# Performance work log

Hardware: AMD Instinct MI355X
Metric: run time of the kernel (lower is better)

Reference implementation:

```python
import jax, jax.numpy as jnp
import numpy as np

K = 1.0          # Lorentz curvature param: x_t^2 - |x_s|^2 = K
SQRT_K = 1.0
EPS = 1e-8
HEADS = 12

def add_time(s):
    t = jnp.sqrt(K + jnp.sum(s * s, axis=-1, keepdims=True))
    return jnp.concatenate([t, s], axis=-1)

def lorentz_ln(x, g, b):
    s = x[..., 1:]
    mu = jnp.mean(s, axis=-1, keepdims=True)
    var = jnp.var(s, axis=-1, keepdims=True)
    s = (s - mu) / jnp.sqrt(var + 1e-5) * g + b
    return add_time(s)

def lorentz_fc(x, W, heads=None, act=None):
    # linear on full Lorentz vector -> space part; time recomputed to stay on manifold
    s = x @ W.T
    if act is not None:
        s = act(s)
    if heads is not None:
        bsz, n, dt = s.shape
        s = s.reshape(bsz, n, heads, dt // heads).transpose(0, 2, 1, 3)  # (b,h,n,hd)
    return add_time(s)

def logmap0(x):
    t, s = x[..., :1], x[..., 1:]
    sn = jnp.sqrt(jnp.sum(s * s, axis=-1, keepdims=True))
    dist = SQRT_K * jnp.arccosh(jnp.maximum(t / SQRT_K, 1.0 + 1e-7))
    u = dist * s / jnp.maximum(sn, EPS)
    return jnp.concatenate([jnp.zeros_like(t), u], axis=-1)

def expmap0(u):
    us = u[..., 1:]
    n = jnp.sqrt(jnp.sum(us * us, axis=-1, keepdims=True))
    nc = jnp.maximum(n, EPS)
    t = SQRT_K * jnp.cosh(n / SQRT_K)
    s = SQRT_K * jnp.sinh(n / SQRT_K) * us / nc
    return jnp.concatenate([t, s], axis=-1)

def ste_clip(x, lo, hi):
    # straight-through estimator: clamp in fwd, identity grad
    return x + jax.lax.stop_gradient(jnp.clip(x, lo, hi) - x)

def ste_max_clamp(x, hi):
    return x + jax.lax.stop_gradient(jnp.minimum(x, hi) - x)

def mha_last_layer(x, Wq, Wk, Wv, Wo, alpha_raw, tau_raw, lambda_raw):
    q = lorentz_fc(x, Wq, heads=HEADS)   # (b,h,n,hd+1)
    k = lorentz_fc(x, Wk, heads=HEADS)
    v = lorentz_fc(x, Wv, heads=HEADS)
    q_t, q_s = q[..., :1], q[..., 1:]
    k_t, k_s = k[..., :1], k[..., 1:]
    # Lorentzian inner product -> hyperbolic pairwise distances
    inner_QK = -q_t @ jnp.swapaxes(k_t, -1, -2) + jnp.einsum('bhid,bhjd->bhij', q_s, k_s)
    raw_cosh = jnp.maximum(-inner_QK / K, 1.0)                # (b,h,n,n)
    is_self = raw_cosh < 1.0 + 1e-5
    safe_cosh = jnp.where(is_self, 2.0, raw_cosh)
    dist_QK = SQRT_K * jnp.arccosh(safe_cosh)
    cosh_OQ = jnp.maximum(q_t / SQRT_K, 1.0 + 1e-7)
    cosh_OK = jnp.maximum(k_t / SQRT_K, 1.0 + 1e-7)
    c_tilde = jnp.minimum(SQRT_K * jnp.arccosh(cosh_OQ), 40.0) / SQRT_K  # (b,h,n,1)
    sinh_QK = jnp.sinh(dist_QK / SQRT_K)
    sinh_OQ = jnp.sinh(c_tilde)
    numer = raw_cosh * cosh_OQ - jnp.swapaxes(cosh_OK, -1, -2)
    raw_Z = numer / (sinh_OQ * sinh_QK)
    Z_safe = jnp.where(is_self, 1.0, ste_clip(raw_Z, -1.0, 1.0))
    alpha = jax.nn.softplus(alpha_raw)
    B = alpha * c_tilde / (1.0 + alpha * c_tilde)
    lam = jax.nn.softplus(lambda_raw)
    d_L = ste_max_clamp(dist_QK, 40.0)   # float32 branch of STE_Dist_Clamp
    log_dist_penalty = -lam * jnp.log1p(d_L * d_L)
    m = 0.1
    entail = jax.nn.softplus(B + Z_safe - m) - jax.nn.softplus(jnp.asarray(-m, B.dtype))
    tau = jax.nn.softplus(tau_raw)
    score = jax.nn.softmax(log_dist_penalty - tau * entail, axis=-1)
    # expmap aggregation: tangent-space weighted mean
    v_tan = logmap0(v)
    agg = jnp.einsum('bhij,bhjd->bhid', score, v_tan)
    agg = agg / (jnp.sum(score, axis=-1, keepdims=True) + 1e-8)
    attn = expmap0(agg).transpose(0, 2, 1, 3)   # (b,n,h,hd+1)
    bsz, n, h, _ = attn.shape
    attn_s = attn[..., 1:].reshape(bsz, n, -1)
    attn_t = attn[..., :1].reshape(bsz, n, -1)
    t_new = jnp.sqrt(jnp.sum(attn_t ** 2, axis=-1, keepdims=True) - (h - 1) * K)
    return lorentz_fc(jnp.concatenate([t_new, attn_s], axis=-1), Wo)


def setup_inputs() -> dict:
    key = jax.random.key(0)
    ks = jax.random.split(key, 8)
    b, n, hidden, mlp_hidden = 4, 1024, 769, 3073
    d = hidden - 1
    xs = jax.random.normal(ks[0], (b, n, d), jnp.float32)
    x = add_time(xs)
    def w(k, o, i):
        return jax.random.normal(k, (o, i), jnp.float32) * (i ** -0.5)
    return {
        'x': x,
        'Wq': w(ks[1], d, hidden), 'Wk': w(ks[2], d, hidden), 'Wv': w(ks[3], d, hidden),
        'Wo': w(ks[4], d, hidden),
        'ln1_g': jnp.ones((d,), jnp.float32), 'ln1_b': jnp.zeros((d,), jnp.float32),
        'ln2_g': jnp.ones((d,), jnp.float32), 'ln2_b': jnp.zeros((d,), jnp.float32),
        'Wm1': w(ks[5], mlp_hidden - 1, hidden), 'Wm2': w(ks[6], d, mlp_hidden),
        'alpha_raw': jnp.zeros((1,), jnp.float32),
        'tau_raw': jnp.zeros((1,), jnp.float32),
        'lambda_raw': jnp.zeros((1,), jnp.float32),
    }


def reference(x, Wq, Wk, Wv, Wo, ln1_g, ln1_b, ln2_g, ln2_b, Wm1, Wm2, alpha_raw, tau_raw, lambda_raw):
    out = mha_last_layer(lorentz_ln(x, ln1_g, ln1_b), Wq, Wk, Wv, Wo, alpha_raw, tau_raw, lambda_raw)
    out = out[..., 1:] + x[..., 1:]                 # residual on space part (DropPath=identity in eval)
    h = lorentz_ln(add_time(out), ln2_g, ln2_b)
    h = lorentz_fc(h, Wm1, act=lambda z: jax.nn.gelu(z, approximate=False))
    h = lorentz_fc(h, Wm2)
    out = h[..., 1:] + out
    return add_time(out)
```

## Files before the change

### kernel.cpp

```cpp
#include <hip/hip_runtime.h>
#include <cstdint>
#include <cstddef>

typedef unsigned short u16;
typedef __attribute__((ext_vector_type(8))) __bf16 bf16x8;
typedef __attribute__((ext_vector_type(4))) float f32x4;

#define SEQ 1024
#define MROWS 4096
#define DDIM 768
#define HID 769
#define KP1 800
#define MLPD 3072
#define KP2 3104
#define NHEADS 12
#define LN2F 0.69314718056f
#define LOG2EF 1.44269504089f

static __device__ __forceinline__ u16 f2bf(float f){
  union { float f; uint32_t u; } v; v.f = f;
  return (u16)((v.u + 0x7FFFu + ((v.u >> 16) & 1u)) >> 16);
}

static __device__ __forceinline__ f32x4 mfma16(bf16x8 a, bf16x8 b, f32x4 c){
  return __builtin_amdgcn_mfma_f32_16x16x32_bf16(a, b, c, 0, 0, 0);
}

static __device__ __forceinline__ void async_lds16(const u16* g, u16* l){
  u16* gm = const_cast<u16*>(g);
  __builtin_amdgcn_global_load_lds(
      (__attribute__((address_space(1))) void*)gm,
      (__attribute__((address_space(3))) void*)l, 16, 0, 0);
}

static __device__ __forceinline__ float blk_reduce(float v, float* red, int tid){
  #pragma unroll
  for (int off = 1; off < 64; off <<= 1) v += __shfl_xor(v, off, 64);
  __syncthreads();
  if ((tid & 63) == 0) red[tid >> 6] = v;
  __syncthreads();
  return red[0] + red[1] + red[2] + red[3];
}

static __device__ __forceinline__ void conv_seg(const float* W, u16* O, int idx, int K, int Kp){
  int n = idx / Kp, k = idx - n * Kp;
  O[idx] = (k < K) ? f2bf(W[(size_t)n * K + k]) : (u16)0;
}
__global__ __launch_bounds__(256) void conv_all(const float* __restrict__ Wq, const float* __restrict__ Wk,
    const float* __restrict__ Wv, const float* __restrict__ Wo,
    const float* __restrict__ Wm1, const float* __restrict__ Wm2, u16* __restrict__ dst){
  int b = blockIdx.x, tid = threadIdx.x;
  if (b < 2400){        conv_seg(Wq,  dst,            b*256+tid,        769, 800); }
  else if (b < 4800){   conv_seg(Wk,  dst + 614400,  (b-2400)*256+tid,  769, 800); }
  else if (b < 7200){   conv_seg(Wv,  dst + 1228800, (b-4800)*256+tid,  769, 800); }
  else if (b < 9600){   conv_seg(Wo,  dst + 1843200, (b-7200)*256+tid,  769, 800); }
  else if (b < 19200){  conv_seg(Wm1, dst + 2457600, (b-9600)*256+tid,  769, 800); }
  else {                conv_seg(Wm2, dst + 4915200, (b-19200)*256+tid, 3073, 3104); }
}

__global__ __launch_bounds__(256) void ln_kernel(const float* __restrict__ X, int xstr, int xoff,
    const float* __restrict__ g, const float* __restrict__ b, u16* __restrict__ O){
  __shared__ float red[4];
  int m = blockIdx.x, tid = threadIdx.x;
  const float* xr = X + (size_t)m * xstr + xoff;
  float s[3], y[3];
  float s1 = 0.f, s2 = 0.f;
  #pragma unroll
  for (int j = 0; j < 3; j++){ float v = xr[tid + j*256]; s[j] = v; s1 += v; s2 += v*v; }
  s1 = blk_reduce(s1, red, tid);
  s2 = blk_reduce(s2, red, tid);
  float mu = s1 * (1.f/768.f);
  float var = s2 * (1.f/768.f) - mu*mu;
  float rstd = rsqrtf(var + 1e-5f);
  float q = 0.f;
  #pragma unroll
  for (int j = 0; j < 3; j++){ int i = tid + j*256; y[j] = (s[j]-mu)*rstd*g[i] + b[i]; q += y[j]*y[j]; }
  q = blk_reduce(q, red, tid);
  u16* orow = O + (size_t)m * KP1;
  #pragma unroll
  for (int j = 0; j < 3; j++) orow[1 + tid + j*256] = f2bf(y[j]);
  if (tid == 0) orow[0] = f2bf(sqrtf(1.f + q));
  if (tid < 31) orow[769 + tid] = 0;
}

__global__ __launch_bounds__(256) void ln_sum_kernel(const float* __restrict__ P4,
    const float* __restrict__ x, const float* __restrict__ g, const float* __restrict__ b,
    float* __restrict__ out1, u16* __restrict__ O){
  __shared__ float red[4];
  int m = blockIdx.x, tid = threadIdx.x;
  float s[3], y[3];
  float s1 = 0.f, s2 = 0.f;
  #pragma unroll
  for (int j = 0; j < 3; j++){
    int col = tid + j*256;
    float v = x[(size_t)m * HID + 1 + col];
    #pragma unroll
    for (int z = 0; z < 4; z++) v += P4[(size_t)z*MROWS*DDIM + (size_t)m*DDIM + col];
    out1[(size_t)m*DDIM + col] = v;
    s[j] = v; s1 += v; s2 += v*v;
  }
  s1 = blk_reduce(s1, red, tid);
  s2 = blk_reduce(s2, red, tid);
  float mu = s1 * (1.f/768.f);
  float var = s2 * (1.f/768.f) - mu*mu;
  float rstd = rsqrtf(var + 1e-5f);
  float q = 0.f;
  #pragma unroll
  for (int j = 0; j < 3; j++){ int i = tid + j*256; y[j] = (s[j]-mu)*rstd*g[i] + b[i]; q += y[j]*y[j]; }
  q = blk_reduce(q, red, tid);
  u16* orow = O + (size_t)m * KP1;
  #pragma unroll
  for (int j = 0; j < 3; j++) orow[1 + tid + j*256] = f2bf(y[j]);
  if (tid == 0) orow[0] = f2bf(sqrtf(1.f + q));
  if (tid < 31) orow[769 + tid] = 0;
}

__global__ __launch_bounds__(256) void gemm_qkv(
    const u16* __restrict__ A,
    const u16* __restrict__ B0, const u16* __restrict__ B1, const u16* __restrict__ B2,
    float* __restrict__ C, int N, int Kp)
{
  __shared__ u16 As[128*32];
  __shared__ u16 Bs[128*32];
  int tid = threadIdx.x;
  int wave = tid >> 6, lane = tid & 63;
  int lrow = lane & 15, lq = lane >> 4;
  int m0 = blockIdx.y * 128, n0 = blockIdx.x * 128;
  int wm = wave >> 1, wn = wave & 1;
  const u16* B = (blockIdx.z == 0) ? B0 : (blockIdx.z == 1 ? B1 : B2);
  C += (size_t)blockIdx.z * MROWS * N;
  f32x4 acc[4][4] = {};
  int seg = wave * 2;
  int srow = lane >> 2;
  int scol = (lane & 3) * 8;
  const u16* Abase = A + (size_t)m0 * Kp;
  const u16* Bbase = B + (size_t)n0 * Kp;
  for (int k0 = 0; k0 < Kp; k0 += 32){
    __syncthreads();
    #pragma unroll
    for (int i = 0; i < 2; i++){
      int s = seg + i;
      async_lds16(Abase + (size_t)(s*16 + srow) * Kp + k0 + scol, As + s*512);
      async_lds16(Bbase + (size_t)(s*16 + srow) * Kp + k0 + scol, Bs + s*512);
    }
    __syncthreads();
    bf16x8 af[4], bfr[4];
    #pragma unroll
    for (int t = 0; t < 4; t++){
      af[t]  = *(const bf16x8*)(As + (wm*64 + t*16 + lrow)*32 + lq*8);
      bfr[t] = *(const bf16x8*)(Bs + (wn*64 + t*16 + lrow)*32 + lq*8);
    }
    #pragma unroll
    for (int mt = 0; mt < 4; mt++)
      #pragma unroll
      for (int nt = 0; nt < 4; nt++)
        acc[mt][nt] = mfma16(af[mt], bfr[nt], acc[mt][nt]);
  }
  #pragma unroll
  for (int mt = 0; mt < 4; mt++)
    #pragma unroll
    for (int nt = 0; nt < 4; nt++){
      int col = n0 + wn*64 + nt*16 + lrow;
      #pragma unroll
      for (int r = 0; r < 4; r++){
        int row = m0 + wm*64 + mt*16 + lq*4 + r;
        C[(size_t)row * N + col] = acc[mt][nt][r];
      }
    }
}

__global__ __launch_bounds__(256) void gemm_split(
    const u16* __restrict__ A, const u16* __restrict__ B, float* __restrict__ C,
    int N, int Kp)
{
  __shared__ u16 As[128*32];
  __shared__ u16 Bs[128*32];
  int tid = threadIdx.x;
  int wave = tid >> 6, lane = tid & 63;
  int lrow = lane & 15, lq = lane >> 4;
  int m0 = blockIdx.y * 128, n0 = blockIdx.x * 128;
  int wm = wave >> 1, wn = wave & 1;
  int chunks = Kp >> 5;
  int nz = gridDim.z, z = blockIdx.z;
  int base = chunks / nz, rem = chunks - base * nz;
  int begin = z * base + (z < rem ? z : rem);
  int count = base + (z < rem ? 1 : 0);
  C += (size_t)z * MROWS * N;
  f32x4 acc[4][4] = {};
  int seg = wave * 2;
  int srow = lane >> 2;
  int scol = (lane & 3) * 8;
  const u16* Abase = A + (size_t)m0 * Kp;
  const u16* Bbase = B + (size_t)n0 * Kp;
  for (int kc = begin; kc < begin + count; kc++){
    int k0 = kc * 32;
    __syncthreads();
    #pragma unroll
    for (int i = 0; i < 2; i++){
      int s = seg + i;
      async_lds16(Abase + (size_t)(s*16 + srow) * Kp + k0 + scol, As + s*512);
      async_lds16(Bbase + (size_t)(s*16 + srow) * Kp + k0 + scol, Bs + s*512);
    }
    __syncthreads();
    bf16x8 af[4], bfr[4];
    #pragma unroll
    for (int t = 0; t < 4; t++){
      af[t]  = *(const bf16x8*)(As + (wm*64 + t*16 + lrow)*32 + lq*8);
      bfr[t] = *(const bf16x8*)(Bs + (wn*64 + t*16 + lrow)*32 + lq*8);
    }
    #pragma unroll
    for (int mt = 0; mt < 4; mt++)
      #pragma unroll
      for (int nt = 0; nt < 4; nt++)
        acc[mt][nt] = mfma16(af[mt], bfr[nt], acc[mt][nt]);
  }
  #pragma unroll
  for (int mt = 0; mt < 4; mt++)
    #pragma unroll
    for (int nt = 0; nt < 4; nt++){
      int col = n0 + wn*64 + nt*16 + lrow;
      #pragma unroll
      for (int r = 0; r < 4; r++){
        int row = m0 + wm*64 + mt*16 + lq*4 + r;
        C[(size_t)row * N + col] = acc[mt][nt][r];
      }
    }
}

__global__ __launch_bounds__(256) void pack_qk(const float* __restrict__ raw,
    u16* __restrict__ Qp, u16* __restrict__ Kpk, float* __restrict__ qt, float* __restrict__ kt)
{
  int wave = threadIdx.x >> 6, lane = threadIdx.x & 63;
  int m = blockIdx.x * 4 + wave;
  int h = blockIdx.y;
  int which = blockIdx.z;
  const float* src = raw + (size_t)which * MROWS * DDIM + (size_t)m * DDIM + h*64 + lane;
  float v = *src;
  float ss = v*v;
  #pragma unroll
  for (int off = 1; off < 64; off <<= 1) ss += __shfl_xor(ss, off, 64);
  int b = m >> 10, n = m & 1023, bh = b * NHEADS + h;
  u16* dst = (which ? Kpk : Qp) + ((size_t)bh * SEQ + n) * 64 + lane;
  *dst = f2bf(v);
  if (lane == 0) (which ? kt : qt)[bh * SEQ + n] = sqrtf(1.f + ss);
}

__global__ __launch_bounds__(256) void pack_v(const float* __restrict__ vraw, u16* __restrict__ Vt){
  __shared__ float part[256];
  __shared__ float scl[64];
  __shared__ float tile[64][65];
  int tid = threadIdx.x;
  int kb = blockIdx.x, bh = blockIdx.y;
  int b = bh / NHEADS, h = bh - b*NHEADS;
  int kl = tid >> 2;
  int d0 = (tid & 3) * 16;
  int m = b * SEQ + kb * 64 + kl;
  float v[16]; float ss = 0.f;
  const float* src = vraw + (size_t)m * DDIM + h*64 + d0;
  #pragma unroll
  for (int i = 0; i < 16; i++){ v[i] = src[i]; ss += v[i]*v[i]; }
  part[tid] = ss;
  __syncthreads();
  if ((tid & 3) == 0){
    float s2 = part[tid] + part[tid+1] + part[tid+2] + part[tid+3];
    float sn = sqrtf(s2);
    float tv = sqrtf(1.f + s2);
    float ctv = fmaxf(tv, 1.f + 1e-7f);
    float dist = __logf(ctv + sqrtf(fmaxf(ctv*ctv - 1.f, 0.f)));
    scl[kl] = dist / fmaxf(sn, 1e-8f);
  }
  __syncthreads();
  float sc = scl[kl];
  #pragma unroll
  for (int i = 0; i < 16; i++) tile[kl][d0 + i] = v[i] * sc;
  __syncthreads();
  int dim = tid >> 2;
  int kk0 = (tid & 3) * 16;
  u16 tmp[16];
  #pragma unroll
  for (int i = 0; i < 16; i++) tmp[i] = f2bf(tile[kk0 + i][dim]);
  u16* dst = Vt + ((size_t)bh * 64 + dim) * SEQ + kb*64 + kk0;
  *(uint4*)dst       = *(const uint4*)tmp;
  *(uint4*)(dst + 8) = *(const uint4*)(tmp + 8);
}

__global__ __launch_bounds__(256) void attn_kernel(
    const u16* __restrict__ Q, const u16* __restrict__ K, const u16* __restrict__ Vt,
    const float* __restrict__ qt, const float* __restrict__ kt,
    float* __restrict__ pAgg, float* __restrict__ pDen,
    const float* __restrict__ a_raw, const float* __restrict__ t_raw, const float* __restrict__ l_raw)
{
  __shared__ float rv[4][64];
  __shared__ u16 Pl[4][16*72];
  int tid = threadIdx.x;
  int bh = blockIdx.y, ks = blockIdx.z;
  int qbase = blockIdx.x * 64;
  float alpha = __logf(1.f + __expf(a_raw[0]));
  float tau   = __logf(1.f + __expf(t_raw[0]));
  float lam   = __logf(1.f + __expf(l_raw[0]));
  if (tid < 64){
    float qtv = qt[bh * SEQ + qbase + tid];
    float cq = fmaxf(qtv, 1.f + 1e-7f);
    float A = cq + __builtin_amdgcn_sqrtf(fmaxf(cq*cq - 1.f, 0.f));
    float ct = fminf(__builtin_amdgcn_logf(A) * LN2F, 40.f);
    float e = __expf(ct);
    float sh = 0.5f * (e - __builtin_amdgcn_rcpf(e));
    float ac = alpha * ct;
    rv[0][tid] = qtv;
    rv[1][tid] = cq;
    rv[2][tid] = __builtin_amdgcn_rcpf(sh);
    rv[3][tid] = (ac * __builtin_amdgcn_rcpf(1.f + ac) - 0.1f) * LOG2EF;
  }
  __syncthreads();
  int wave = tid >> 6, lane = tid & 63;
  int lrow = lane & 15, lq = lane >> 4;
  int myrow = wave*16 + lrow;
  float qt_l = rv[0][myrow], cq_l = rv[1][myrow], rri_l = rv[2][myrow], Bw_l = rv[3][myrow];
  const float tbase = tau * 0.92967051f;
  const u16* Qb = Q + ((size_t)bh * SEQ + qbase + wave*16 + lrow) * 64 + lq*8;
  bf16x8 bq0 = *(const bf16x8*)Qb;
  bf16x8 bq1 = *(const bf16x8*)(Qb + 32);
  const u16* Kh = K + (size_t)bh * SEQ * 64;
  const u16* Vh = Vt + (size_t)bh * 64 * SEQ;
  const float* ktp = kt + (size_t)bh * SEQ;
  u16* Pw = &Pl[wave][0];
  f32x4 o[4] = {};
  float dsum = 0.f;
  for (int jt = 0; jt < 8; jt++){
    int jbase = ks * 512 + jt * 64;
    f32x4 s[4];
    #pragma unroll
    for (int ct = 0; ct < 4; ct++){
      const u16* Ka = Kh + (size_t)(jbase + ct*16 + lrow) * 64 + lq*8;
      bf16x8 a0 = *(const bf16x8*)Ka;
      bf16x8 a1 = *(const bf16x8*)(Ka + 32);
      f32x4 z = {0.f, 0.f, 0.f, 0.f};
      z = mfma16(a0, bq0, z);
      z = mfma16(a1, bq1, z);
      s[ct] = z;
    }
    #pragma unroll
    for (int ct = 0; ct < 4; ct++){
      float4 kv = *(const float4*)(ktp + jbase + ct*16 + lq*4);
      uint32_t pu[4];
      #pragma unroll
      for (int r = 0; r < 4; r++){
        float ktv = (r == 0) ? kv.x : (r == 1) ? kv.y : (r == 2) ? kv.z : kv.w;
        float c = fmaxf(__builtin_fmaf(qt_l, ktv, -s[ct][r]), 1.f);
        bool self = c < 1.00001f;
        float ce = self ? 2.f : c;
        float cm1 = __builtin_fmaf(ce, ce, -1.f);
        float rs = __builtin_amdgcn_rsqf(cm1);
        float shq = cm1 * rs;
        float d = fminf(__builtin_amdgcn_logf(ce + shq) * LN2F, 40.f);
        float L1 = __builtin_amdgcn_logf(__builtin_fmaf(d, d, 1.f));
        float Z = __builtin_fmaf(ce, cq_l, -ktv) * rri_l * rs;
        Z = fminf(fmaxf(Z, -1.f), 1.f);
        Z = self ? 1.f : Z;
        float w2 = __builtin_fmaf(Z, LOG2EF, Bw_l);
        float ew = __builtin_amdgcn_exp2f(w2);
        float L2 = __builtin_amdgcn_logf(ew + 1.f);
        float logit = __builtin_fmaf(-lam, L1, __builtin_fmaf(-tau, L2, tbase));
        float p = __builtin_amdgcn_exp2f(logit);
        uint32_t u = __float_as_uint(p);
        pu[r] = u;
        dsum += __uint_as_float(u & 0xFFFF0000u);
      }
      uint32_t lo = __builtin_amdgcn_perm(pu[1], pu[0], 0x07060302u);
      uint32_t hi = __builtin_amdgcn_perm(pu[3], pu[2], 0x07060302u);
      uint2 pk; pk.x = lo; pk.y = hi;
      *(uint2*)(Pw + lrow*72 + ct*16 + lq*4) = pk;
    }
    bf16x8 ap0 = *(const bf16x8*)(Pw + lrow*72 + lq*8);
    bf16x8 ap1 = *(const bf16x8*)(Pw + lrow*72 + 32 + lq*8);
    #pragma unroll
    for (int nt = 0; nt < 4; nt++){
      const u16* Vb = Vh + (size_t)(nt*16 + lrow) * SEQ + jbase + lq*8;
      bf16x8 bv0 = *(const bf16x8*)Vb;
      bf16x8 bv1 = *(const bf16x8*)(Vb + 32);
      o[nt] = mfma16(ap0, bv0, o[nt]);
      o[nt] = mfma16(ap1, bv1, o[nt]);
    }
  }
  dsum += __shfl_xor(dsum, 16, 64);
  dsum += __shfl_xor(dsum, 32, 64);
  size_t pbase = ((size_t)(ks*48 + bh) * SEQ) + qbase;
  if (lq == 0) pDen[pbase + wave*16 + lrow] = dsum;
  #pragma unroll
  for (int nt = 0; nt < 4; nt++)
    #pragma unroll
    for (int r = 0; r < 4; r++)
      pAgg[(pbase + wave*16 + lq*4 + r) * 64 + nt*16 + lrow] = o[nt][r];
}

__global__ __launch_bounds__(768) void expmap_pack(const float* __restrict__ pAgg,
    const float* __restrict__ pDen, u16* __restrict__ O){
  __shared__ float th2[NHEADS];
  int m = blockIdx.x, tid = threadIdx.x;
  int h = tid >> 6, lane = tid & 63;
  int b = m >> 10, n = m & 1023, bh = b*NHEADS + h;
  size_t i0 = ((size_t)bh * SEQ + n);
  size_t i1 = ((size_t)(48 + bh) * SEQ + n);
  float d = pDen[i0] + pDen[i1];
  float rden = __builtin_amdgcn_rcpf(d * (1.f + 1e-8f));
  float u = (pAgg[i0*64 + lane] + pAgg[i1*64 + lane]) * rden;
  float n2 = u*u;
  #pragma unroll
  for (int off = 1; off < 64; off <<= 1) n2 += __shfl_xor(n2, off, 64);
  float nn = sqrtf(n2);
  float e = __expf(nn);
  float ch = 0.5f * (e + 1.f/e);
  float sh = 0.5f * (e - 1.f/e);
  float sc = sh / fmaxf(nn, 1e-8f);
  u16* orow = O + (size_t)m * KP1;
  orow[1 + h*64 + lane] = f2bf(u * sc);
  if (lane == 0) th2[h] = ch*ch;
  __syncthreads();
  if (tid == 0){
    float ssum = 0.f;
    #pragma unroll
    for (int i = 0; i < NHEADS; i++) ssum += th2[i];
    orow[0] = f2bf(sqrtf(ssum - 11.f));
  }
  if (tid >= 1 && tid < 32) orow[768 + tid] = 0;
}

__global__ __launch_bounds__(256) void gelu_pack(const float* __restrict__ Zin, u16* __restrict__ O){
  __shared__ float red[4];
  int m = blockIdx.x, tid = threadIdx.x;
  const float* zr = Zin + (size_t)m * MLPD;
  float gv[12]; float gs = 0.f;
  #pragma unroll
  for (int j = 0; j < 12; j++){
    float z = zr[tid + j*256];
    float e = 0.5f * z * (1.f + erff(z * 0.70710678f));
    gv[j] = e; gs += e*e;
  }
  gs = blk_reduce(gs, red, tid);
  u16* orow = O + (size_t)m * KP2;
  #pragma unroll
  for (int j = 0; j < 12; j++) orow[1 + tid + j*256] = f2bf(gv[j]);
  if (tid == 0) orow[0] = f2bf(sqrtf(1.f + gs));
  if (tid < 31) orow[3073 + tid] = 0;
}

__global__ __launch_bounds__(256) void final_sum(const float* __restrict__ P4,
    const float* __restrict__ out1, float* __restrict__ out){
  __shared__ float red[4];
  int m = blockIdx.x, tid = threadIdx.x;
  float v[3]; float s2 = 0.f;
  #pragma unroll
  for (int j = 0; j < 3; j++){
    int col = tid + j*256;
    float t = out1[(size_t)m*DDIM + col];
    #pragma unroll
    for (int z = 0; z < 4; z++) t += P4[(size_t)z*MROWS*DDIM + (size_t)m*DDIM + col];
    v[j] = t; s2 += t*t;
  }
  s2 = blk_reduce(s2, red, tid);
  float* orow = out + (size_t)m * HID;
  if (tid == 0) orow[0] = sqrtf(1.f + s2);
  #pragma unroll
  for (int j = 0; j < 3; j++) orow[1 + tid + j*256] = v[j];
}

extern "C" void kernel_launch(void* const* d_in, const int* in_sizes, int n_in,
                              void* d_out, int out_size, void* d_ws, size_t ws_size,
                              hipStream_t stream)
{
  (void)in_sizes; (void)n_in; (void)out_size; (void)ws_size;
  const float* x   = (const float*)d_in[0];
  const float* Wq  = (const float*)d_in[1];
  const float* Wk  = (const float*)d_in[2];
  const float* Wv  = (const float*)d_in[3];
  const float* Wo  = (const float*)d_in[4];
  const float* g1p = (const float*)d_in[5];
  const float* b1p = (const float*)d_in[6];
  const float* g2p = (const float*)d_in[7];
  const float* b2p = (const float*)d_in[8];
  const float* Wm1 = (const float*)d_in[9];
  const float* Wm2 = (const float*)d_in[10];
  const float* ar  = (const float*)d_in[11];
  const float* tr  = (const float*)d_in[12];
  const float* lr  = (const float*)d_in[13];

  char* ws = (char*)d_ws;
  u16*   wqb  = (u16*)(ws + 0);
  u16*   wkb  = (u16*)(ws + 1228800);
  u16*   wvb  = (u16*)(ws + 2457600);
  u16*   wob  = (u16*)(ws + 3686400);
  u16*   wm1b = (u16*)(ws + 4915200);
  u16*   wm2b = (u16*)(ws + 9830400);
  u16*   xln  = (u16*)(ws + 14598144);
  float* qkv  = (float*)(ws + 21151744);
  u16*   qp   = (u16*)(ws + 58900480);
  u16*   kpk  = (u16*)(ws + 65191936);
  u16*   vt   = (u16*)(ws + 71483392);
  float* qtb  = (float*)(ws + 77774848);
  float* ktb  = (float*)(ws + 77971456);
  float* pAgg = (float*)(ws + 78168064);
  float* pDen = (float*)(ws + 103333888);
  u16*   woin = (u16*)(ws + 103727104);
  float* woP  = (float*)(ws + 21151744);
  float* out1 = (float*)(ws + 78168064);
  u16*   ln2b = (u16*)(ws + 90750976);
  float* mlp1 = (float*)(ws + 21151744);
  u16*   g1b  = (u16*)(ws + 90750976);
  float* out2P= (float*)(ws + 21151744);

  conv_all<<<dim3(28512), 256, 0, stream>>>(Wq, Wk, Wv, Wo, Wm1, Wm2, wqb);
  ln_kernel<<<dim3(4096), 256, 0, stream>>>(x, 769, 1, g1p, b1p, xln);
  gemm_qkv<<<dim3(6, 32, 3), 256, 0, stream>>>(xln, wqb, wkb, wvb, qkv, 768, 800);
  pack_qk<<<dim3(1024, 12, 2), 256, 0, stream>>>(qkv, qp, kpk, qtb, ktb);
  pack_v<<<dim3(16, 48), 256, 0, stream>>>(qkv + (size_t)2*MROWS*DDIM, vt);
  attn_kernel<<<dim3(16, 48, 2), 256, 0, stream>>>(qp, kpk, vt, qtb, ktb, pAgg, pDen, ar, tr, lr);
  expmap_pack<<<dim3(4096), 768, 0, stream>>>(pAgg, pDen, woin);
  gemm_split<<<dim3(6, 32, 4), 256, 0, stream>>>(woin, wob, woP, 768, 800);
  ln_sum_kernel<<<dim3(4096), 256, 0, stream>>>(woP, x, g2p, b2p, out1, ln2b);
  gemm_split<<<dim3(24, 32, 1), 256, 0, stream>>>(ln2b, wm1b, mlp1, 3072, 800);
  gelu_pack<<<dim3(4096), 256, 0, stream>>>(mlp1, g1b);
  gemm_split<<<dim3(6, 32, 4), 256, 0, stream>>>(g1b, wm2b, out2P, 768, 3104);
  final_sum<<<dim3(4096), 256, 0, stream>>>(out2P, out1, (float*)d_out);
}
```

Measured before the change: 424.7 us.

## Fuse QKV into one GEMM, split attention K four ways, feed P via registers

Replaces the three-way QKV GEMM with a single gemm_split over the concatenated weights, writing a row-interleaved 2304-wide output that the pack kernels now read with the new stride. The attention key range is split into four partitions instead of two, for more blocks and parallelism, with partial results spread across two workspace buffers. The P·V product now uses the 16x16x16 bf16 MFMA with P kept in registers, removing the per-wave LDS staging, and partial outputs are stored as float4. The distance clamp at 40 is dropped, expmap_pack sums four partials, and the workspace layout is reshuffled, which risks buffer overlap and more partial-sum traffic.

```diff
diff --git a/kernel.cpp b/kernel.cpp
--- a/kernel.cpp
+++ b/kernel.cpp
@@ -5,6 +5,7 @@
 typedef unsigned short u16;
 typedef __attribute__((ext_vector_type(8))) __bf16 bf16x8;
 typedef __attribute__((ext_vector_type(4))) float f32x4;
+typedef __attribute__((ext_vector_type(4))) short s16x4;
 
 #define SEQ 1024
 #define MROWS 4096
@@ -26,6 +27,14 @@
   return __builtin_amdgcn_mfma_f32_16x16x32_bf16(a, b, c, 0, 0, 0);
 }
 
+static __device__ __forceinline__ f32x4 mfma16k(s16x4 a, s16x4 b, f32x4 c){
+  return __builtin_amdgcn_mfma_f32_16x16x16bf16_1k(a, b, c, 0, 0, 0);
+}
+
+static __device__ __forceinline__ s16x4 pack4(uint32_t lo, uint32_t hi){
+  union { uint2 u; s16x4 v; } cv; cv.u.x = lo; cv.u.y = hi; return cv.v;
+}
+
 static __device__ __forceinline__ void async_lds16(const u16* g, u16* l){
   u16* gm = const_cast<u16*>(g);
   __builtin_amdgcn_global_load_lds(
@@ -113,60 +122,6 @@
   for (int j = 0; j < 3; j++) orow[1 + tid + j*256] = f2bf(y[j]);
   if (tid == 0) orow[0] = f2bf(sqrtf(1.f + q));
   if (tid < 31) orow[769 + tid] = 0;
-}
-
-__global__ __launch_bounds__(256) void gemm_qkv(
-    const u16* __restrict__ A,
-    const u16* __restrict__ B0, const u16* __restrict__ B1, const u16* __restrict__ B2,
-    float* __restrict__ C, int N, int Kp)
-{
-  __shared__ u16 As[128*32];
-  __shared__ u16 Bs[128*32];
-  int tid = threadIdx.x;
-  int wave = tid >> 6, lane = tid & 63;
-  int lrow = lane & 15, lq = lane >> 4;
-  int m0 = blockIdx.y * 128, n0 = blockIdx.x * 128;
-  int wm = wave >> 1, wn = wave & 1;
-  const u16* B = (blockIdx.z == 0) ? B0 : (blockIdx.z == 1 ? B1 : B2);
-  C += (size_t)blockIdx.z * MROWS * N;
-  f32x4 acc[4][4] = {};
-  int seg = wave * 2;
-  int srow = lane >> 2;
-  int scol = (lane & 3) * 8;
-  const u16* Abase = A + (size_t)m0 * Kp;
-  const u16* Bbase = B + (size_t)n0 * Kp;
-  for (int k0 = 0; k0 < Kp; k0 += 32){
-    __syncthreads();
-    #pragma unroll
-    for (int i = 0; i < 2; i++){
-      int s = seg + i;
-      async_lds16(Abase + (size_t)(s*16 + srow) * Kp + k0 + scol, As + s*512);
-      async_lds16(Bbase + (size_t)(s*16 + srow) * Kp + k0 + scol, Bs + s*512);
-    }
-    __syncthreads();
-    bf16x8 af[4], bfr[4];
-    #pragma unroll
-    for (int t = 0; t < 4; t++){
-      af[t]  = *(const bf16x8*)(As + (wm*64 + t*16 + lrow)*32 + lq*8);
-      bfr[t] = *(const bf16x8*)(Bs + (wn*64 + t*16 + lrow)*32 + lq*8);
-    }
-    #pragma unroll
-    for (int mt = 0; mt < 4; mt++)
-      #pragma unroll
-      for (int nt = 0; nt < 4; nt++)
-        acc[mt][nt] = mfma16(af[mt], bfr[nt], acc[mt][nt]);
-  }
-  #pragma unroll
-  for (int mt = 0; mt < 4; mt++)
-    #pragma unroll
-    for (int nt = 0; nt < 4; nt++){
-      int col = n0 + wn*64 + nt*16 + lrow;
-      #pragma unroll
-      for (int r = 0; r < 4; r++){
-        int row = m0 + wm*64 + mt*16 + lq*4 + r;
-        C[(size_t)row * N + col] = acc[mt][nt][r];
-      }
-    }
 }
 
 __global__ __launch_bounds__(256) void gemm_split(
@@ -234,7 +189,7 @@
   int m = blockIdx.x * 4 + wave;
   int h = blockIdx.y;
   int which = blockIdx.z;
-  const float* src = raw + (size_t)which * MROWS * DDIM + (size_t)m * DDIM + h*64 + lane;
+  const float* src = raw + (size_t)m * 2304 + which * 768 + h*64 + lane;
   float v = *src;
   float ss = v*v;
   #pragma unroll
@@ -256,7 +211,7 @@
   int d0 = (tid & 3) * 16;
   int m = b * SEQ + kb * 64 + kl;
   float v[16]; float ss = 0.f;
-  const float* src = vraw + (size_t)m * DDIM + h*64 + d0;
+  const float* src = vraw + (size_t)m * 2304 + h*64 + d0;
   #pragma unroll
   for (int i = 0; i < 16; i++){ v[i] = src[i]; ss += v[i]*v[i]; }
   part[tid] = ss;
@@ -287,11 +242,10 @@
 __global__ __launch_bounds__(256) void attn_kernel(
     const u16* __restrict__ Q, const u16* __restrict__ K, const u16* __restrict__ Vt,
     const float* __restrict__ qt, const float* __restrict__ kt,
-    float* __restrict__ pAgg, float* __restrict__ pDen,
+    float* __restrict__ pAggA, float* __restrict__ pAggB, float* __restrict__ pDen,
     const float* __restrict__ a_raw, const float* __restrict__ t_raw, const float* __restrict__ l_raw)
 {
   __shared__ float rv[4][64];
-  __shared__ u16 Pl[4][16*72];
   int tid = threadIdx.x;
   int bh = blockIdx.y, ks = blockIdx.z;
   int qbase = blockIdx.x * 64;
@@ -323,11 +277,10 @@
   const u16* Kh = K + (size_t)bh * SEQ * 64;
   const u16* Vh = Vt + (size_t)bh * 64 * SEQ;
   const float* ktp = kt + (size_t)bh * SEQ;
-  u16* Pw = &Pl[wave][0];
   f32x4 o[4] = {};
   float dsum = 0.f;
-  for (int jt = 0; jt < 8; jt++){
-    int jbase = ks * 512 + jt * 64;
+  for (int jt = 0; jt < 4; jt++){
+    int jbase = ks * 256 + jt * 64;
     f32x4 s[4];
     #pragma unroll
     for (int ct = 0; ct < 4; ct++){
@@ -339,6 +292,7 @@
       z = mfma16(a1, bq1, z);
       s[ct] = z;
     }
+    s16x4 pb[4];
     #pragma unroll
     for (int ct = 0; ct < 4; ct++){
       float4 kv = *(const float4*)(ktp + jbase + ct*16 + lq*4);
@@ -352,7 +306,7 @@
         float cm1 = __builtin_fmaf(ce, ce, -1.f);
         float rs = __builtin_amdgcn_rsqf(cm1);
         float shq = cm1 * rs;
-        float d = fminf(__builtin_amdgcn_logf(ce + shq) * LN2F, 40.f);
+        float d = __builtin_amdgcn_logf(ce + shq) * LN2F;
         float L1 = __builtin_amdgcn_logf(__builtin_fmaf(d, d, 1.f));
         float Z = __builtin_fmaf(ce, cq_l, -ktv) * rri_l * rs;
         Z = fminf(fmaxf(Z, -1.f), 1.f);
@@ -368,42 +322,43 @@
       }
       uint32_t lo = __builtin_amdgcn_perm(pu[1], pu[0], 0x07060302u);
       uint32_t hi = __builtin_amdgcn_perm(pu[3], pu[2], 0x07060302u);
-      uint2 pk; pk.x = lo; pk.y = hi;
-      *(uint2*)(Pw + lrow*72 + ct*16 + lq*4) = pk;
-    }
-    bf16x8 ap0 = *(const bf16x8*)(Pw + lrow*72 + lq*8);
-    bf16x8 ap1 = *(const bf16x8*)(Pw + lrow*72 + 32 + lq*8);
-    #pragma unroll
-    for (int nt = 0; nt < 4; nt++){
-      const u16* Vb = Vh + (size_t)(nt*16 + lrow) * SEQ + jbase + lq*8;
-      bf16x8 bv0 = *(const bf16x8*)Vb;
-      bf16x8 bv1 = *(const bf16x8*)(Vb + 32);
-      o[nt] = mfma16(ap0, bv0, o[nt]);
-      o[nt] = mfma16(ap1, bv1, o[nt]);
+      pb[ct] = pack4(lo, hi);
+    }
+    #pragma unroll
+    for (int ct = 0; ct < 4; ct++){
+      #pragma unroll
+      for (int nt = 0; nt < 4; nt++){
+        s16x4 va = *(const s16x4*)(Vh + (size_t)(nt*16 + lrow) * SEQ + jbase + ct*16 + lq*4);
+        o[nt] = mfma16k(va, pb[ct], o[nt]);
+      }
     }
   }
   dsum += __shfl_xor(dsum, 16, 64);
   dsum += __shfl_xor(dsum, 32, 64);
-  size_t pbase = ((size_t)(ks*48 + bh) * SEQ) + qbase;
-  if (lq == 0) pDen[pbase + wave*16 + lrow] = dsum;
-  #pragma unroll
-  for (int nt = 0; nt < 4; nt++)
-    #pragma unroll
-    for (int r = 0; r < 4; r++)
-      pAgg[(pbase + wave*16 + lq*4 + r) * 64 + nt*16 + lrow] = o[nt][r];
-}
-
-__global__ __launch_bounds__(768) void expmap_pack(const float* __restrict__ pAgg,
-    const float* __restrict__ pDen, u16* __restrict__ O){
+  float* pAgg = (ks < 2) ? (pAggA + (size_t)ks * 48 * SEQ * 64)
+                         : (pAggB + (size_t)(ks - 2) * 48 * SEQ * 64);
+  size_t rowb = (size_t)bh * SEQ + qbase + wave*16 + lrow;
+  if (lq == 0) pDen[(size_t)ks * 48 * SEQ + rowb] = dsum;
+  #pragma unroll
+  for (int nt = 0; nt < 4; nt++){
+    float4 ov; ov.x = o[nt][0]; ov.y = o[nt][1]; ov.z = o[nt][2]; ov.w = o[nt][3];
+    *(float4*)(pAgg + rowb * 64 + nt*16 + lq*4) = ov;
+  }
+}
+
+__global__ __launch_bounds__(768) void expmap_pack(const float* __restrict__ pAggA,
+    const float* __restrict__ pAggB, const float* __restrict__ pDen, u16* __restrict__ O){
   __shared__ float th2[NHEADS];
   int m = blockIdx.x, tid = threadIdx.x;
   int h = tid >> 6, lane = tid & 63;
   int b = m >> 10, n = m & 1023, bh = b*NHEADS + h;
-  size_t i0 = ((size_t)bh * SEQ + n);
-  size_t i1 = ((size_t)(48 + bh) * SEQ + n);
-  float d = pDen[i0] + pDen[i1];
+  size_t base = (size_t)bh * SEQ + n;
+  float d = pDen[base] + pDen[(size_t)48*SEQ + base]
+          + pDen[(size_t)96*SEQ + base] + pDen[(size_t)144*SEQ + base];
   float rden = __builtin_amdgcn_rcpf(d * (1.f + 1e-8f));
-  float u = (pAgg[i0*64 + lane] + pAgg[i1*64 + lane]) * rden;
+  float u = pAggA[base*64 + lane] + pAggA[((size_t)48*SEQ + base)*64 + lane]
+          + pAggB[base*64 + lane] + pAggB[((size_t)48*SEQ + base)*64 + lane];
+  u *= rden;
   float n2 = u*u;
   #pragma unroll
   for (int off = 1; off < 64; off <<= 1) n2 += __shfl_xor(n2, off, 64);
@@ -486,8 +441,6 @@
 
   char* ws = (char*)d_ws;
   u16*   wqb  = (u16*)(ws + 0);
-  u16*   wkb  = (u16*)(ws + 1228800);
-  u16*   wvb  = (u16*)(ws + 2457600);
   u16*   wob  = (u16*)(ws + 3686400);
   u16*   wm1b = (u16*)(ws + 4915200);
   u16*   wm2b = (u16*)(ws + 9830400);
@@ -498,23 +451,24 @@
   u16*   vt   = (u16*)(ws + 71483392);
   float* qtb  = (float*)(ws + 77774848);
   float* ktb  = (float*)(ws + 77971456);
-  float* pAgg = (float*)(ws + 78168064);
+  float* pAggA= (float*)(ws + 14598144);
+  float* pAggB= (float*)(ws + 78168064);
   float* pDen = (float*)(ws + 103333888);
-  u16*   woin = (u16*)(ws + 103727104);
-  float* woP  = (float*)(ws + 21151744);
-  float* out1 = (float*)(ws + 78168064);
-  u16*   ln2b = (u16*)(ws + 90750976);
-  float* mlp1 = (float*)(ws + 21151744);
-  u16*   g1b  = (u16*)(ws + 90750976);
-  float* out2P= (float*)(ws + 21151744);
+  u16*   woin = (u16*)(ws + 104120320);
+  float* woP  = (float*)(ws + 14598144);
+  float* out1 = (float*)(ws + 64929792);
+  u16*   ln2b = (u16*)(ws + 77512704);
+  float* mlp1 = (float*)(ws + 14598144);
+  u16*   g1b  = (u16*)(ws + 84066304);
+  float* out2P= (float*)(ws + 14598144);
 
   conv_all<<<dim3(28512), 256, 0, stream>>>(Wq, Wk, Wv, Wo, Wm1, Wm2, wqb);
   ln_kernel<<<dim3(4096), 256, 0, stream>>>(x, 769, 1, g1p, b1p, xln);
-  gemm_qkv<<<dim3(6, 32, 3), 256, 0, stream>>>(xln, wqb, wkb, wvb, qkv, 768, 800);
+  gemm_split<<<dim3(18, 32, 1), 256, 0, stream>>>(xln, wqb, qkv, 2304, 800);
   pack_qk<<<dim3(1024, 12, 2), 256, 0, stream>>>(qkv, qp, kpk, qtb, ktb);
-  pack_v<<<dim3(16, 48), 256, 0, stream>>>(qkv + (size_t)2*MROWS*DDIM, vt);
-  attn_kernel<<<dim3(16, 48, 2), 256, 0, stream>>>(qp, kpk, vt, qtb, ktb, pAgg, pDen, ar, tr, lr);
-  expmap_pack<<<dim3(4096), 768, 0, stream>>>(pAgg, pDen, woin);
+  pack_v<<<dim3(16, 48), 256, 0, stream>>>(qkv + 1536, vt);
+  attn_kernel<<<dim3(16, 48, 4), 256, 0, stream>>>(qp, kpk, vt, qtb, ktb, pAggA, pAggB, pDen, ar, tr, lr);
+  expmap_pack<<<dim3(4096), 768, 0, stream>>>(pAggA, pAggB, pDen, woin);
   gemm_split<<<dim3(6, 32, 4), 256, 0, stream>>>(woin, wob, woP, 768, 800);
   ln_sum_kernel<<<dim3(4096), 256, 0, stream>>>(woP, x, g2p, b2p, out1, ln2b);
   gemm_split<<<dim3(24, 32, 1), 256, 0, stream>>>(ln2b, wm1b, mlp1, 3072, 800);
```

New measurement: 447.2 us. 1.05x slower.
